# Optimization experiments

Hardware: AMD Instinct MI355X
Metric: run time of the kernel (lower is better)

## Reference

```python
import jax, jax.numpy as jnp
import numpy as np

BC, N, F, D = 16, 2048, 128, 128
N_EDGES = 65536
NEG_INF = -1e16
LEAK = 0.1


def setup_inputs() -> dict:
    key = jax.random.key(0)
    k_h, k_w, k_r, k_c = jax.random.split(key, 4)
    h = jax.random.normal(k_h, (BC, N, F), dtype=jnp.float32)
    # xavier_normal with gain 1.414
    w_std = 1.414 * np.sqrt(2.0 / (F + D))
    W = jax.random.normal(k_w, (F, D), dtype=jnp.float32) * w_std
    row = jax.random.randint(k_r, (N_EDGES,), 0, N, dtype=jnp.int64)
    col = jax.random.randint(k_c, (N_EDGES,), 0, N, dtype=jnp.int64)
    return {"h": h, "W": W, "row": row, "col": col}


def reference(h, W, row, col):
    bc, n, f = h.shape
    # z = h @ W : [bc, N, D]
    z = jnp.einsum("bnf,fd->bnd", h, W)
    # dense inner-product attention scores [bc, N, N]
    att = jnp.einsum("bnd,bmd->bnm", z, z)
    # leaky_relu(0.1)
    att = jnp.where(att > 0, att, LEAK * att)
    # sparse adjacency mask built from COO indices
    mask = jnp.zeros((n, n), dtype=att.dtype).at[row, col].set(1.0)
    att = att * mask[None, :, :]
    # masked_fill where value == 0 (non-edges, and incidental exact zeros)
    att = jnp.where(att == 0.0, NEG_INF, att)
    att = jax.nn.softmax(att, axis=2)
    # aggregate: [bc, N, N] @ [bc, N, D]
    return jnp.einsum("bnm,bmd->bnd", att, z)
```

## Files before the change

### kernel.cpp

```cpp
#include <hip/hip_runtime.h>

#define BC 16
#define NN 2048
#define FF 128
#define DD 128
#define NEDGES 65536
#define NEG_INF -1e16f
#define LEAK 0.1f
#define CAPR 128

__global__ void __launch_bounds__(256) zedge_kernel(const float* __restrict__ h,
                                                    const float* __restrict__ W,
                                                    float* __restrict__ z,
                                                    const int* __restrict__ row,
                                                    const int* __restrict__ col,
                                                    unsigned int* __restrict__ mask) {
    const int tid = threadIdx.x;
    const int blk = blockIdx.x;

    if (blk < 256) {
        const int e = blk * 256 + tid;
        const unsigned int key = (unsigned int)row[e] * NN + (unsigned int)col[e];
        atomicOr(&mask[key >> 5], 1u << (key & 31u));
        return;
    }

    __shared__ float hs[32][FF];
    const size_t row0 = (size_t)(blk - 256) * 32;
    const float4* hv = (const float4*)(h + row0 * FF);
    float4* hsv = (float4*)&hs[0][0];
#pragma unroll
    for (int i = 0; i < 4; ++i) hsv[tid + 256 * i] = hv[tid + 256 * i];
    __syncthreads();

    const int c0 = (tid & 31) * 4;
    const int r0 = (tid >> 5) * 4;
    float acc[4][4] = {};
    for (int f = 0; f < FF; f += 4) {
        float4 a[4], bb[4];
#pragma unroll
        for (int r = 0; r < 4; ++r) a[r] = *(const float4*)&hs[r0 + r][f];
#pragma unroll
        for (int k = 0; k < 4; ++k) bb[k] = *(const float4*)&W[(f + k) * DD + c0];
#pragma unroll
        for (int r = 0; r < 4; ++r) {
            acc[r][0] += a[r].x * bb[0].x + a[r].y * bb[1].x + a[r].z * bb[2].x + a[r].w * bb[3].x;
            acc[r][1] += a[r].x * bb[0].y + a[r].y * bb[1].y + a[r].z * bb[2].y + a[r].w * bb[3].y;
            acc[r][2] += a[r].x * bb[0].z + a[r].y * bb[1].z + a[r].z * bb[2].z + a[r].w * bb[3].z;
            acc[r][3] += a[r].x * bb[0].w + a[r].y * bb[1].w + a[r].z * bb[2].w + a[r].w * bb[3].w;
        }
    }
#pragma unroll
    for (int r = 0; r < 4; ++r)
        *(float4*)&z[(row0 + r0 + r) * DD + c0] =
            make_float4(acc[r][0], acc[r][1], acc[r][2], acc[r][3]);
}

__global__ void __launch_bounds__(256) csr_kernel(const unsigned int* __restrict__ mask,
                                                  unsigned short* __restrict__ hits_g,
                                                  int* __restrict__ deg) {
    const int tid = threadIdx.x, wv = tid >> 6, ln = tid & 63;
    const int n = blockIdx.x * 4 + wv;
    unsigned int bits = mask[n * 64 + ln];
    const int cnt = __popc(bits);
    int pre = cnt;
#pragma unroll
    for (int off = 1; off <= 32; off <<= 1) {
        const int t = __shfl_up(pre, off, 64);
        if (ln >= off) pre += t;
    }
    if (ln == 63) deg[n] = pre;
    int slot = pre - cnt;
    while (bits) {
        const int bit = __ffs(bits) - 1;
        bits &= bits - 1;
        if (slot < CAPR) hits_g[n * CAPR + slot] = (unsigned short)(ln * 32 + bit);
        ++slot;
    }
}

__global__ void __launch_bounds__(256) gat_kernel(const float* __restrict__ z,
                                                  const unsigned short* __restrict__ hits_g,
                                                  const int* __restrict__ deg,
                                                  float* __restrict__ out) {
    const int tid = threadIdx.x, wv = tid >> 6, ln = tid & 63;
    const int blk = blockIdx.x;
    const int b = ((blk & 7) << 1) | (wv & 1);
    const int n = ((blk >> 3) << 1) | (wv >> 1);
    const int eq = ln >> 3, hq = ln & 7;

    const float* zb = z + ((size_t)b << 18);
    const int nh = min(deg[n], CAPR);
    const unsigned short* hrow = hits_g + n * CAPR;

    const float4* znp = (const float4*)(zb + ((size_t)n << 7) + (hq << 4));
    const float4 a0 = znp[0], a1 = znp[1], a2 = znp[2], a3 = znp[3];

    float m = NEG_INF, l = 0.f;
    float4 acc0 = make_float4(0.f, 0.f, 0.f, 0.f), acc1 = acc0, acc2 = acc0, acc3 = acc0;

#pragma unroll 2
    for (int c0 = 0; c0 < nh; c0 += 8) {
        const int e = c0 + eq;
        const int he = hrow[min(e, nh - 1)];
        const float4* zc = (const float4*)(zb + ((size_t)he << 7) + (hq << 4));
        const float4 v0 = zc[0], v1 = zc[1], v2 = zc[2], v3 = zc[3];
        float pt = a0.x * v0.x + a0.y * v0.y + a0.z * v0.z + a0.w * v0.w
                 + a1.x * v1.x + a1.y * v1.y + a1.z * v1.z + a1.w * v1.w
                 + a2.x * v2.x + a2.y * v2.y + a2.z * v2.z + a2.w * v2.w
                 + a3.x * v3.x + a3.y * v3.y + a3.z * v3.z + a3.w * v3.w;
        pt += __shfl_xor(pt, 1, 64);
        pt += __shfl_xor(pt, 2, 64);
        pt += __shfl_xor(pt, 4, 64);
        float sv = pt > 0.f ? pt : LEAK * pt;
        if (sv == 0.f || e >= nh) sv = NEG_INF;

        const float mnew = fmaxf(m, sv);
        const float alpha = __expf(m - mnew);
        const float pr = __expf(sv - mnew);
        l = l * alpha + pr;
        acc0.x = acc0.x * alpha + pr * v0.x; acc0.y = acc0.y * alpha + pr * v0.y;
        acc0.z = acc0.z * alpha + pr * v0.z; acc0.w = acc0.w * alpha + pr * v0.w;
        acc1.x = acc1.x * alpha + pr * v1.x; acc1.y = acc1.y * alpha + pr * v1.y;
        acc1.z = acc1.z * alpha + pr * v1.z; acc1.w = acc1.w * alpha + pr * v1.w;
        acc2.x = acc2.x * alpha + pr * v2.x; acc2.y = acc2.y * alpha + pr * v2.y;
        acc2.z = acc2.z * alpha + pr * v2.z; acc2.w = acc2.w * alpha + pr * v2.w;
        acc3.x = acc3.x * alpha + pr * v3.x; acc3.y = acc3.y * alpha + pr * v3.y;
        acc3.z = acc3.z * alpha + pr * v3.z; acc3.w = acc3.w * alpha + pr * v3.w;
        m = mnew;
    }

    float M = m;
#pragma unroll
    for (int off = 8; off <= 32; off <<= 1) M = fmaxf(M, __shfl_xor(M, off, 64));

    if (nh > 0 && M > 0.5f * NEG_INF) {
        const float al = __expf(m - M);
        l *= al;
        acc0.x *= al; acc0.y *= al; acc0.z *= al; acc0.w *= al;
        acc1.x *= al; acc1.y *= al; acc1.z *= al; acc1.w *= al;
        acc2.x *= al; acc2.y *= al; acc2.z *= al; acc2.w *= al;
        acc3.x *= al; acc3.y *= al; acc3.z *= al; acc3.w *= al;
#pragma unroll
        for (int off = 8; off <= 32; off <<= 1) {
            l += __shfl_xor(l, off, 64);
            acc0.x += __shfl_xor(acc0.x, off, 64); acc0.y += __shfl_xor(acc0.y, off, 64);
            acc0.z += __shfl_xor(acc0.z, off, 64); acc0.w += __shfl_xor(acc0.w, off, 64);
            acc1.x += __shfl_xor(acc1.x, off, 64); acc1.y += __shfl_xor(acc1.y, off, 64);
            acc1.z += __shfl_xor(acc1.z, off, 64); acc1.w += __shfl_xor(acc1.w, off, 64);
            acc2.x += __shfl_xor(acc2.x, off, 64); acc2.y += __shfl_xor(acc2.y, off, 64);
            acc2.z += __shfl_xor(acc2.z, off, 64); acc2.w += __shfl_xor(acc2.w, off, 64);
            acc3.x += __shfl_xor(acc3.x, off, 64); acc3.y += __shfl_xor(acc3.y, off, 64);
            acc3.z += __shfl_xor(acc3.z, off, 64); acc3.w += __shfl_xor(acc3.w, off, 64);
        }
        const float inv = 1.f / l;
        acc0.x *= inv; acc0.y *= inv; acc0.z *= inv; acc0.w *= inv;
        acc1.x *= inv; acc1.y *= inv; acc1.z *= inv; acc1.w *= inv;
        acc2.x *= inv; acc2.y *= inv; acc2.z *= inv; acc2.w *= inv;
        acc3.x *= inv; acc3.y *= inv; acc3.z *= inv; acc3.w *= inv;
    } else {
        acc0 = make_float4(0.f, 0.f, 0.f, 0.f); acc1 = acc0; acc2 = acc0; acc3 = acc0;
        for (int mm = 0; mm < NN; ++mm) {
            const float4* zr = (const float4*)(zb + ((size_t)mm << 7) + (hq << 4));
            const float4 t0 = zr[0], t1 = zr[1], t2 = zr[2], t3 = zr[3];
            acc0.x += t0.x; acc0.y += t0.y; acc0.z += t0.z; acc0.w += t0.w;
            acc1.x += t1.x; acc1.y += t1.y; acc1.z += t1.z; acc1.w += t1.w;
            acc2.x += t2.x; acc2.y += t2.y; acc2.z += t2.z; acc2.w += t2.w;
            acc3.x += t3.x; acc3.y += t3.y; acc3.z += t3.z; acc3.w += t3.w;
        }
        const float s = 1.f / NN;
        acc0.x *= s; acc0.y *= s; acc0.z *= s; acc0.w *= s;
        acc1.x *= s; acc1.y *= s; acc1.z *= s; acc1.w *= s;
        acc2.x *= s; acc2.y *= s; acc2.z *= s; acc2.w *= s;
        acc3.x *= s; acc3.y *= s; acc3.z *= s; acc3.w *= s;
    }

    if (eq < 4) {
        float4 o = acc0;
        if (eq == 1) o = acc1;
        if (eq == 2) o = acc2;
        if (eq == 3) o = acc3;
        *(float4*)(out + (((size_t)b * NN + n) << 7) + (hq << 4) + (eq << 2)) = o;
    }
}

extern "C" void kernel_launch(void* const* d_in, const int* in_sizes, int n_in,
                              void* d_out, int out_size, void* d_ws, size_t ws_size,
                              hipStream_t stream) {
    const float* h = (const float*)d_in[0];
    const float* W = (const float*)d_in[1];
    const int* row = (const int*)d_in[2];
    const int* col = (const int*)d_in[3];
    float* out = (float*)d_out;

    char* ws = (char*)d_ws;
    float* z = (float*)ws;
    unsigned int* mask = (unsigned int*)(ws + (size_t)16 * 1024 * 1024);
    unsigned short* hits_g = (unsigned short*)(ws + (size_t)16 * 1024 * 1024 + 512 * 1024);
    int* deg = (int*)(ws + (size_t)17 * 1024 * 1024);

    hipMemsetAsync(mask, 0, (size_t)NN * NN / 8, stream);
    zedge_kernel<<<1280, 256, 0, stream>>>(h, W, z, row, col, mask);
    csr_kernel<<<NN / 4, 256, 0, stream>>>(mask, hits_g, deg);
    gat_kernel<<<(BC * NN) / 4, 256, 0, stream>>>(z, hits_g, deg, out);
}
```

Before: 149.8 us.

## Fuse projection, CSR build and attention into one cooperative persistent kernel

Replaces the three launches (z projection plus mask build, CSR compaction, attention aggregation) with a single cooperative kernel that uses grid-wide syncs between phases. The attention phase now has each wave handle two batches per node to reuse the neighbour index loads, and it uses a lazy softmax rescale that only updates the running max when a new score exceeds it by a threshold. The aim is to remove launch gaps and redundant index traffic. The cost is grid.sync overhead, a fixed persistent grid size, and a per-lane max that can lag behind the true maximum. The original three-kernel path is kept as a fallback if the cooperative launch fails.

```diff
diff --git a/kernel.cpp b/kernel.cpp
--- a/kernel.cpp
+++ b/kernel.cpp
@@ -1,4 +1,7 @@
 #include <hip/hip_runtime.h>
+#include <hip/hip_cooperative_groups.h>
+
+namespace cg = cooperative_groups;
 
 #define BC 16
 #define NN 2048
@@ -8,6 +11,218 @@
 #define NEG_INF -1e16f
 #define LEAK 0.1f
 #define CAPR 128
+#define THRS 20.0f
+
+__device__ __forceinline__ float dot16(const float4& a0, const float4& a1, const float4& a2, const float4& a3,
+                                       const float4& v0, const float4& v1, const float4& v2, const float4& v3) {
+    return a0.x * v0.x + a0.y * v0.y + a0.z * v0.z + a0.w * v0.w
+         + a1.x * v1.x + a1.y * v1.y + a1.z * v1.z + a1.w * v1.w
+         + a2.x * v2.x + a2.y * v2.y + a2.z * v2.z + a2.w * v2.w
+         + a3.x * v3.x + a3.y * v3.y + a3.z * v3.z + a3.w * v3.w;
+}
+__device__ __forceinline__ void sc4(float4& c, float s) { c.x *= s; c.y *= s; c.z *= s; c.w *= s; }
+__device__ __forceinline__ void fma4(float4& c, float p, const float4& v) {
+    c.x += p * v.x; c.y += p * v.y; c.z += p * v.z; c.w += p * v.w;
+}
+__device__ __forceinline__ void add4(float4& c, const float4& v) {
+    c.x += v.x; c.y += v.y; c.z += v.z; c.w += v.w;
+}
+__device__ __forceinline__ void red4(float4& c, int off) {
+    c.x += __shfl_xor(c.x, off, 64); c.y += __shfl_xor(c.y, off, 64);
+    c.z += __shfl_xor(c.z, off, 64); c.w += __shfl_xor(c.w, off, 64);
+}
+
+__global__ void __launch_bounds__(256, 4)
+gat_fused(const float* __restrict__ h, const float* __restrict__ W,
+          const int* __restrict__ row, const int* __restrict__ col,
+          float* __restrict__ z, unsigned int* __restrict__ mask,
+          unsigned short* __restrict__ hits_g, int* __restrict__ deg,
+          float* __restrict__ out, int nb) {
+    const int tid = threadIdx.x;
+    const int blk = blockIdx.x;
+    const int wv = tid >> 6, ln = tid & 63;
+    cg::grid_group grid = cg::this_grid();
+    __shared__ float hs[32][FF];
+
+    for (int v = blk; v < 256 + (BC * NN) / 32; v += nb) {
+        if (v < 256) {
+            const int e = v * 256 + tid;
+            const unsigned int key = (unsigned int)row[e] * NN + (unsigned int)col[e];
+            atomicOr(&mask[key >> 5], 1u << (key & 31u));
+        } else {
+            const size_t row0 = (size_t)(v - 256) * 32;
+            const float4* hv = (const float4*)(h + row0 * FF);
+            float4* hsv = (float4*)&hs[0][0];
+#pragma unroll
+            for (int i = 0; i < 4; ++i) hsv[tid + 256 * i] = hv[tid + 256 * i];
+            __syncthreads();
+            const int cc0 = (tid & 31) * 4;
+            const int rr0 = (tid >> 5) * 4;
+            float acc[4][4] = {};
+            for (int f = 0; f < FF; f += 4) {
+                float4 a[4], bb[4];
+#pragma unroll
+                for (int r = 0; r < 4; ++r) a[r] = *(const float4*)&hs[rr0 + r][f];
+#pragma unroll
+                for (int k = 0; k < 4; ++k) bb[k] = *(const float4*)&W[(f + k) * DD + cc0];
+#pragma unroll
+                for (int r = 0; r < 4; ++r) {
+                    acc[r][0] += a[r].x * bb[0].x + a[r].y * bb[1].x + a[r].z * bb[2].x + a[r].w * bb[3].x;
+                    acc[r][1] += a[r].x * bb[0].y + a[r].y * bb[1].y + a[r].z * bb[2].y + a[r].w * bb[3].y;
+                    acc[r][2] += a[r].x * bb[0].z + a[r].y * bb[1].z + a[r].z * bb[2].z + a[r].w * bb[3].z;
+                    acc[r][3] += a[r].x * bb[0].w + a[r].y * bb[1].w + a[r].z * bb[2].w + a[r].w * bb[3].w;
+                }
+            }
+#pragma unroll
+            for (int r = 0; r < 4; ++r)
+                *(float4*)&z[(row0 + rr0 + r) * DD + cc0] =
+                    make_float4(acc[r][0], acc[r][1], acc[r][2], acc[r][3]);
+            __syncthreads();
+        }
+    }
+    grid.sync();
+
+    for (int v = blk; v < NN / 4; v += nb) {
+        const int n = v * 4 + wv;
+        unsigned int bits = mask[n * 64 + ln];
+        const int cnt = __popc(bits);
+        int pre = cnt;
+#pragma unroll
+        for (int off = 1; off <= 32; off <<= 1) {
+            const int t = __shfl_up(pre, off, 64);
+            if (ln >= off) pre += t;
+        }
+        if (ln == 63) deg[n] = pre;
+        int slot = pre - cnt;
+        while (bits) {
+            const int bit = __ffs(bits) - 1;
+            bits &= bits - 1;
+            if (slot < CAPR) hits_g[n * CAPR + slot] = (unsigned short)(ln * 32 + bit);
+            ++slot;
+        }
+    }
+    grid.sync();
+
+    const int eq = ln >> 3, hq = ln & 7;
+    const int doff = hq << 4;
+    const int stride = nb << 2;
+    for (int t = (blk << 2) | wv; t < 16384; t += stride) {
+        const int bp = (t >> 2) & 7;
+        const int n = ((t >> 5) << 2) | (t & 3);
+        const float* zb0 = z + ((size_t)bp << 19);
+        const float* zb1 = zb0 + (1 << 18);
+        const int nh = min(deg[n], CAPR);
+        const unsigned short* hrow = hits_g + n * CAPR;
+
+        const float4* zn0 = (const float4*)(zb0 + ((size_t)n << 7) + doff);
+        const float4* zn1 = (const float4*)(zb1 + ((size_t)n << 7) + doff);
+        const float4 a00 = zn0[0], a01 = zn0[1], a02 = zn0[2], a03 = zn0[3];
+        const float4 a10 = zn1[0], a11 = zn1[1], a12 = zn1[2], a13 = zn1[3];
+
+        float m0 = NEG_INF, l0 = 0.f, m1 = NEG_INF, l1 = 0.f;
+        float4 c00 = make_float4(0.f, 0.f, 0.f, 0.f), c01 = c00, c02 = c00, c03 = c00;
+        float4 c10 = c00, c11 = c00, c12 = c00, c13 = c00;
+
+#pragma unroll 1
+        for (int e0 = 0; e0 < nh; e0 += 8) {
+            const int e = e0 + eq;
+            const int he = hrow[min(e, nh - 1)];
+            const float4* p0 = (const float4*)(zb0 + ((size_t)he << 7) + doff);
+            const float4* p1 = (const float4*)(zb1 + ((size_t)he << 7) + doff);
+            const float4 v00 = p0[0], v01 = p0[1], v02 = p0[2], v03 = p0[3];
+            const float4 v10 = p1[0], v11 = p1[1], v12 = p1[2], v13 = p1[3];
+
+            float pt0 = dot16(a00, a01, a02, a03, v00, v01, v02, v03);
+            float pt1 = dot16(a10, a11, a12, a13, v10, v11, v12, v13);
+            pt0 += __shfl_xor(pt0, 1, 64);  pt1 += __shfl_xor(pt1, 1, 64);
+            pt0 += __shfl_xor(pt0, 2, 64);  pt1 += __shfl_xor(pt1, 2, 64);
+            pt0 += __shfl_xor(pt0, 4, 64);  pt1 += __shfl_xor(pt1, 4, 64);
+
+            float sv0 = pt0 > 0.f ? pt0 : LEAK * pt0;
+            float sv1 = pt1 > 0.f ? pt1 : LEAK * pt1;
+            const bool pad = e >= nh;
+            if (sv0 == 0.f || pad) sv0 = NEG_INF;
+            if (sv1 == 0.f || pad) sv1 = NEG_INF;
+
+            if (__any((sv0 - m0 > THRS) | (sv1 - m1 > THRS))) {
+                const float mn0 = fmaxf(m0, sv0), mn1 = fmaxf(m1, sv1);
+                const float al0 = __expf(m0 - mn0), al1 = __expf(m1 - mn1);
+                m0 = mn0; m1 = mn1;
+                l0 *= al0; l1 *= al1;
+                sc4(c00, al0); sc4(c01, al0); sc4(c02, al0); sc4(c03, al0);
+                sc4(c10, al1); sc4(c11, al1); sc4(c12, al1); sc4(c13, al1);
+            }
+            const float pr0 = __expf(sv0 - m0), pr1 = __expf(sv1 - m1);
+            l0 += pr0; l1 += pr1;
+            fma4(c00, pr0, v00); fma4(c10, pr1, v10);
+            fma4(c01, pr0, v01); fma4(c11, pr1, v11);
+            fma4(c02, pr0, v02); fma4(c12, pr1, v12);
+            fma4(c03, pr0, v03); fma4(c13, pr1, v13);
+        }
+
+        float M0 = m0, M1 = m1;
+#pragma unroll
+        for (int off = 8; off <= 32; off <<= 1) {
+            M0 = fmaxf(M0, __shfl_xor(M0, off, 64));
+            M1 = fmaxf(M1, __shfl_xor(M1, off, 64));
+        }
+        const bool ok0 = (nh > 0) && (M0 > 0.5f * NEG_INF);
+        const bool ok1 = (nh > 0) && (M1 > 0.5f * NEG_INF);
+        if (ok0) {
+            const float al = __expf(m0 - M0);
+            l0 *= al; sc4(c00, al); sc4(c01, al); sc4(c02, al); sc4(c03, al);
+        }
+        if (ok1) {
+            const float al = __expf(m1 - M1);
+            l1 *= al; sc4(c10, al); sc4(c11, al); sc4(c12, al); sc4(c13, al);
+        }
+#pragma unroll
+        for (int off = 8; off <= 32; off <<= 1) {
+            l0 += __shfl_xor(l0, off, 64); l1 += __shfl_xor(l1, off, 64);
+            red4(c00, off); red4(c01, off); red4(c02, off); red4(c03, off);
+            red4(c10, off); red4(c11, off); red4(c12, off); red4(c13, off);
+        }
+        if (ok0) {
+            const float inv = 1.f / l0;
+            sc4(c00, inv); sc4(c01, inv); sc4(c02, inv); sc4(c03, inv);
+        } else {
+            c00 = make_float4(0.f, 0.f, 0.f, 0.f); c01 = c00; c02 = c00; c03 = c00;
+            for (int mm = 0; mm < NN; ++mm) {
+                const float4* zr = (const float4*)(zb0 + ((size_t)mm << 7) + doff);
+                add4(c00, zr[0]); add4(c01, zr[1]); add4(c02, zr[2]); add4(c03, zr[3]);
+            }
+            const float s = 1.f / NN;
+            sc4(c00, s); sc4(c01, s); sc4(c02, s); sc4(c03, s);
+        }
+        if (ok1) {
+            const float inv = 1.f / l1;
+            sc4(c10, inv); sc4(c11, inv); sc4(c12, inv); sc4(c13, inv);
+        } else {
+            c10 = make_float4(0.f, 0.f, 0.f, 0.f); c11 = c10; c12 = c10; c13 = c10;
+            for (int mm = 0; mm < NN; ++mm) {
+                const float4* zr = (const float4*)(zb1 + ((size_t)mm << 7) + doff);
+                add4(c10, zr[0]); add4(c11, zr[1]); add4(c12, zr[2]); add4(c13, zr[3]);
+            }
+            const float s = 1.f / NN;
+            sc4(c10, s); sc4(c11, s); sc4(c12, s); sc4(c13, s);
+        }
+
+        const int b0 = bp << 1;
+        if (eq < 4) {
+            float4 o = c00;
+            if (eq == 1) o = c01;
+            if (eq == 2) o = c02;
+            if (eq == 3) o = c03;
+            *(float4*)(out + (((size_t)b0 * NN + n) << 7) + doff + (eq << 2)) = o;
+        } else {
+            float4 o = c10;
+            if (eq == 5) o = c11;
+            if (eq == 6) o = c12;
+            if (eq == 7) o = c13;
+            *(float4*)(out + (((size_t)(b0 + 1) * NN + n) << 7) + doff + ((eq - 4) << 2)) = o;
+        }
+    }
+}
 
 __global__ void __launch_bounds__(256) zedge_kernel(const float* __restrict__ h,
                                                     const float* __restrict__ W,
@@ -17,14 +232,12 @@
                                                     unsigned int* __restrict__ mask) {
     const int tid = threadIdx.x;
     const int blk = blockIdx.x;
-
     if (blk < 256) {
         const int e = blk * 256 + tid;
         const unsigned int key = (unsigned int)row[e] * NN + (unsigned int)col[e];
         atomicOr(&mask[key >> 5], 1u << (key & 31u));
         return;
     }
-
     __shared__ float hs[32][FF];
     const size_t row0 = (size_t)(blk - 256) * 32;
     const float4* hv = (const float4*)(h + row0 * FF);
@@ -32,7 +245,6 @@
 #pragma unroll
     for (int i = 0; i < 4; ++i) hsv[tid + 256 * i] = hv[tid + 256 * i];
     __syncthreads();
-
     const int c0 = (tid & 31) * 4;
     const int r0 = (tid >> 5) * 4;
     float acc[4][4] = {};
@@ -88,33 +300,25 @@
     const int b = ((blk & 7) << 1) | (wv & 1);
     const int n = ((blk >> 3) << 1) | (wv >> 1);
     const int eq = ln >> 3, hq = ln & 7;
-
     const float* zb = z + ((size_t)b << 18);
     const int nh = min(deg[n], CAPR);
     const unsigned short* hrow = hits_g + n * CAPR;
-
     const float4* znp = (const float4*)(zb + ((size_t)n << 7) + (hq << 4));
     const float4 a0 = znp[0], a1 = znp[1], a2 = znp[2], a3 = znp[3];
-
     float m = NEG_INF, l = 0.f;
     float4 acc0 = make_float4(0.f, 0.f, 0.f, 0.f), acc1 = acc0, acc2 = acc0, acc3 = acc0;
-
 #pragma unroll 2
     for (int c0 = 0; c0 < nh; c0 += 8) {
         const int e = c0 + eq;
         const int he = hrow[min(e, nh - 1)];
         const float4* zc = (const float4*)(zb + ((size_t)he << 7) + (hq << 4));
         const float4 v0 = zc[0], v1 = zc[1], v2 = zc[2], v3 = zc[3];
-        float pt = a0.x * v0.x + a0.y * v0.y + a0.z * v0.z + a0.w * v0.w
-                 + a1.x * v1.x + a1.y * v1.y + a1.z * v1.z + a1.w * v1.w
-                 + a2.x * v2.x + a2.y * v2.y + a2.z * v2.z + a2.w * v2.w
-                 + a3.x * v3.x + a3.y * v3.y + a3.z * v3.z + a3.w * v3.w;
+        float pt = dot16(a0, a1, a2, a3, v0, v1, v2, v3);
         pt += __shfl_xor(pt, 1, 64);
         pt += __shfl_xor(pt, 2, 64);
         pt += __shfl_xor(pt, 4, 64);
         float sv = pt > 0.f ? pt : LEAK * pt;
         if (sv == 0.f || e >= nh) sv = NEG_INF;
-
         const float mnew = fmaxf(m, sv);
         const float alpha = __expf(m - mnew);
         const float pr = __expf(sv - mnew);
@@ -129,52 +333,29 @@
         acc3.z = acc3.z * alpha + pr * v3.z; acc3.w = acc3.w * alpha + pr * v3.w;
         m = mnew;
     }
-
     float M = m;
 #pragma unroll
     for (int off = 8; off <= 32; off <<= 1) M = fmaxf(M, __shfl_xor(M, off, 64));
-
     if (nh > 0 && M > 0.5f * NEG_INF) {
         const float al = __expf(m - M);
         l *= al;
-        acc0.x *= al; acc0.y *= al; acc0.z *= al; acc0.w *= al;
-        acc1.x *= al; acc1.y *= al; acc1.z *= al; acc1.w *= al;
-        acc2.x *= al; acc2.y *= al; acc2.z *= al; acc2.w *= al;
-        acc3.x *= al; acc3.y *= al; acc3.z *= al; acc3.w *= al;
+        sc4(acc0, al); sc4(acc1, al); sc4(acc2, al); sc4(acc3, al);
 #pragma unroll
         for (int off = 8; off <= 32; off <<= 1) {
             l += __shfl_xor(l, off, 64);
-            acc0.x += __shfl_xor(acc0.x, off, 64); acc0.y += __shfl_xor(acc0.y, off, 64);
-            acc0.z += __shfl_xor(acc0.z, off, 64); acc0.w += __shfl_xor(acc0.w, off, 64);
-            acc1.x += __shfl_xor(acc1.x, off, 64); acc1.y += __shfl_xor(acc1.y, off, 64);
-            acc1.z += __shfl_xor(acc1.z, off, 64); acc1.w += __shfl_xor(acc1.w, off, 64);
-            acc2.x += __shfl_xor(acc2.x, off, 64); acc2.y += __shfl_xor(acc2.y, off, 64);
-            acc2.z += __shfl_xor(acc2.z, off, 64); acc2.w += __shfl_xor(acc2.w, off, 64);
-            acc3.x += __shfl_xor(acc3.x, off, 64); acc3.y += __shfl_xor(acc3.y, off, 64);
-            acc3.z += __shfl_xor(acc3.z, off, 64); acc3.w += __shfl_xor(acc3.w, off, 64);
+            red4(acc0, off); red4(acc1, off); red4(acc2, off); red4(acc3, off);
         }
         const float inv = 1.f / l;
-        acc0.x *= inv; acc0.y *= inv; acc0.z *= inv; acc0.w *= inv;
-        acc1.x *= inv; acc1.y *= inv; acc1.z *= inv; acc1.w *= inv;
-        acc2.x *= inv; acc2.y *= inv; acc2.z *= inv; acc2.w *= inv;
-        acc3.x *= inv; acc3.y *= inv; acc3.z *= inv; acc3.w *= inv;
+        sc4(acc0, inv); sc4(acc1, inv); sc4(acc2, inv); sc4(acc3, inv);
     } else {
         acc0 = make_float4(0.f, 0.f, 0.f, 0.f); acc1 = acc0; acc2 = acc0; acc3 = acc0;
         for (int mm = 0; mm < NN; ++mm) {
             const float4* zr = (const float4*)(zb + ((size_t)mm << 7) + (hq << 4));
-            const float4 t0 = zr[0], t1 = zr[1], t2 = zr[2], t3 = zr[3];
-            acc0.x += t0.x; acc0.y += t0.y; acc0.z += t0.z; acc0.w += t0.w;
-            acc1.x += t1.x; acc1.y += t1.y; acc1.z += t1.z; acc1.w += t1.w;
-            acc2.x += t2.x; acc2.y += t2.y; acc2.z += t2.z; acc2.w += t2.w;
-            acc3.x += t3.x; acc3.y += t3.y; acc3.z += t3.z; acc3.w += t3.w;
+            add4(acc0, zr[0]); add4(acc1, zr[1]); add4(acc2, zr[2]); add4(acc3, zr[3]);
         }
         const float s = 1.f / NN;
-        acc0.x *= s; acc0.y *= s; acc0.z *= s; acc0.w *= s;
-        acc1.x *= s; acc1.y *= s; acc1.z *= s; acc1.w *= s;
-        acc2.x *= s; acc2.y *= s; acc2.z *= s; acc2.w *= s;
-        acc3.x *= s; acc3.y *= s; acc3.z *= s; acc3.w *= s;
-    }
-
+        sc4(acc0, s); sc4(acc1, s); sc4(acc2, s); sc4(acc3, s);
+    }
     if (eq < 4) {
         float4 o = acc0;
         if (eq == 1) o = acc1;
@@ -199,7 +380,30 @@
     unsigned short* hits_g = (unsigned short*)(ws + (size_t)16 * 1024 * 1024 + 512 * 1024);
     int* deg = (int*)(ws + (size_t)17 * 1024 * 1024);
 
+    static int nb = 0;
+    static int coop_bad = 0;
+    if (nb == 0) {
+        int per_cu = 0;
+        if (hipOccupancyMaxActiveBlocksPerMultiprocessor(
+                &per_cu, reinterpret_cast<const void*>(gat_fused), 256, 0) != hipSuccess ||
+            per_cu <= 0)
+            per_cu = 4;
+        long g = (long)per_cu * 256;
+        if (g > 2048) g = 2048;
+        nb = (int)(g & ~7L);
+        if (nb < 8) nb = 8;
+    }
+
     hipMemsetAsync(mask, 0, (size_t)NN * NN / 8, stream);
+
+    if (!coop_bad) {
+        void* kargs[] = {(void*)&h, (void*)&W, (void*)&row, (void*)&col, (void*)&z,
+                         (void*)&mask, (void*)&hits_g, (void*)&deg, (void*)&out, (void*)&nb};
+        hipError_t err = hipLaunchCooperativeKernel(
+            reinterpret_cast<const void*>(gat_fused), dim3(nb), dim3(256), kargs, 0, stream);
+        if (err == hipSuccess) return;
+        coop_bad = 1;
+    }
     zedge_kernel<<<1280, 256, 0, stream>>>(h, W, z, row, col, mask);
     csr_kernel<<<NN / 4, 256, 0, stream>>>(mask, hits_g, deg);
     gat_kernel<<<(BC * NN) / 4, 256, 0, stream>>>(z, hits_g, deg, out);
```

After: 332.7 us. 122% more time.
